# Kernel tuning notes

Measured on AMD Instinct MI355X. Metric: run time of the kernel, lower is better.

Reference implementation:

```python
import jax, jax.numpy as jnp
import numpy as np

CHUNK = 400
L = 50          # encoder kernel and stride
JUMP = CHUNK // L  # 8 new frames per streaming step
N = 128         # encoder feature dim
B = 128         # bottleneck dim
H = 512         # TCN hidden dim
K = 3           # depthwise kernel size
R, X = 2, 7     # repeats x blocks, dilations 2^0..2^6
BUF = 516       # ring buffer length: JUMP + 2*sum(dilations)*R = 8 + 508
EPS = 1e-8


def setup_inputs() -> dict:
    key = jax.random.key(0)
    ks = jax.random.split(key, 16)
    nb = R * X
    w = lambda i, shape: jax.random.normal(ks[i], shape, jnp.float32) * 0.05
    return dict(
        mixture=jax.random.normal(ks[0], (1, 2, CHUNK), jnp.float32),
        encoder_buffer=jax.random.uniform(ks[1], (1, N, BUF), dtype=jnp.float32),
        layernorm_buffer=jax.random.normal(ks[2], (1, B, BUF), jnp.float32),
        W_enc=w(3, (N, 2, L)),              # encoder Conv1d(2->N, k=L, s=L)
        ln_g=jnp.ones((N,), jnp.float32),    # channelwise LayerNorm affine
        ln_b=jnp.zeros((N,), jnp.float32),
        W_bn=w(4, (B, N)),                   # bottleneck 1x1 conv
        blk_w1=w(5, (nb, H, B)),             # per-block pointwise in
        blk_p1=jnp.full((nb,), 0.25, jnp.float32),
        blk_g1=jnp.ones((nb, H), jnp.float32),
        blk_b1=jnp.zeros((nb, H), jnp.float32),
        blk_dw=w(6, (nb, H, K)),             # depthwise dilated conv
        blk_p2=jnp.full((nb,), 0.25, jnp.float32),
        blk_g2=jnp.ones((nb, H), jnp.float32),
        blk_b2=jnp.zeros((nb, H), jnp.float32),
        blk_w2=w(7, (nb, B, H)),             # per-block pointwise out
        W_mask=w(8, (N, B)),                 # mask 1x1 conv (C=1 source)
        W_dec=w(9, (L, N)),                  # decoder basis Linear(N->L)
    )


def _cln(x, g, b):
    # channelwise LayerNorm: normalize over channel dim per time frame. x: [1,C,T]
    mu = jnp.mean(x, axis=1, keepdims=True)
    var = jnp.var(x, axis=1, keepdims=True)
    return g[None, :, None] * (x - mu) * jax.lax.rsqrt(var + EPS) + b[None, :, None]


def _prelu(x, a):
    return jnp.where(x >= 0, x, a * x)


def _dwconv(x, w, d):
    # valid dilated depthwise conv. x: [1,H,T], w: [H,K] -> [1,H,T-(K-1)*d]
    return jax.lax.conv_general_dilated(
        x, w[:, None, :], window_strides=(1,), padding='VALID',
        rhs_dilation=(d,), feature_group_count=H,
        dimension_numbers=('NCH', 'OIH', 'NCH'))


def reference(mixture, encoder_buffer, layernorm_buffer, W_enc, ln_g, ln_b, W_bn,
              blk_w1, blk_p1, blk_g1, blk_b1, blk_dw, blk_p2, blk_g2, blk_b2,
              blk_w2, W_mask, W_dec):
    # --- encoder: Conv1d(2->N, k=L, s=L) + ReLU -> JUMP new frames, ring-shift buffer
    enc = jax.nn.relu(jax.lax.conv_general_dilated(
        mixture, W_enc, window_strides=(L,), padding='VALID',
        dimension_numbers=('NCH', 'OIH', 'NCH')))          # [1,N,JUMP]
    encoder_buffer = jnp.concatenate([encoder_buffer[:, :, JUMP:], enc], axis=2)

    # --- separator front-end (network[0:2]): cLN + bottleneck 1x1, per-frame causal
    ln_new = jnp.einsum('oc,bct->bot', W_bn, _cln(enc, ln_g, ln_b))  # [1,B,JUMP]
    layernorm_buffer = jnp.concatenate([layernorm_buffer[:, :, JUMP:], ln_new], axis=2)

    # --- TCN (network[2]): valid causal dilated blocks, each shrinks time by 2*d
    x = layernorm_buffer                                   # [1,B,516]
    for i in range(R * X):
        d = 2 ** (i % X)
        y = jnp.einsum('hc,bct->bht', blk_w1[i], x)
        y = _cln(_prelu(y, blk_p1[i]), blk_g1[i], blk_b1[i])
        y = _dwconv(y, blk_dw[i], d)                       # time -= (K-1)*d
        y = _cln(_prelu(y, blk_p2[i]), blk_g2[i], blk_b2[i])
        y = jnp.einsum('ch,bht->bct', blk_w2[i], y)
        x = x[:, :, (K - 1) * d:] + y                      # residual on trailing frames
    # x: [1,B,JUMP]

    # --- mask conv (network[3]) + ReLU, reshape to [1,C=1,N,JUMP]
    mask = jax.nn.relu(jnp.einsum('nc,bct->bnt', W_mask, x)).reshape(1, 1, N, JUMP)

    # --- decoder: mask the newest JUMP encoder frames, basis Linear(N->L), stride=L
    src_w = encoder_buffer[:, None, :, -JUMP:] * mask      # [1,1,N,JUMP]
    est_source = jnp.einsum('ln,bcnt->bctl', W_dec, src_w).reshape(1, 1, JUMP * L)
    return est_source, encoder_buffer, layernorm_buffer
```

## Files before the change

kernel.cpp:

```cpp
#include <hip/hip_runtime.h>

#define CHUNK 400
#define LWIN 50
#define JUMP 8
#define NCH 128
#define BCH 128
#define HCH 512
#define NBLK 14
#define BUF 516
#define SHIFT 508
#define EPSV 1e-8f
#define NWG 136

typedef float f4v __attribute__((ext_vector_type(4)));

__device__ __forceinline__ void cstore4(float* p, float4 v) {
    f4v t = {v.x, v.y, v.z, v.w};
    asm volatile("global_store_dwordx4 %0, %1, off sc0 sc1"
                 :: "v"(p), "v"(t) : "memory");
}
__device__ __forceinline__ float4 cload4(const float* p) {
    f4v t;
    asm volatile("global_load_dwordx4 %0, %1, off sc0 sc1\n\ts_waitcnt vmcnt(0)"
                 : "=v"(t) : "v"(p) : "memory");
    return make_float4(t.x, t.y, t.z, t.w);
}
__device__ __forceinline__ void cload4x3(float4& a, float4& b, float4& c,
        const float* pa, const float* pb, const float* pc) {
    f4v ta, tb, tc;
    asm volatile("global_load_dwordx4 %0, %3, off sc0 sc1\n\t"
                 "global_load_dwordx4 %1, %4, off sc0 sc1\n\t"
                 "global_load_dwordx4 %2, %5, off sc0 sc1\n\t"
                 "s_waitcnt vmcnt(0)"
                 : "=&v"(ta), "=&v"(tb), "=&v"(tc)
                 : "v"(pa), "v"(pb), "v"(pc) : "memory");
    a = make_float4(ta.x, ta.y, ta.z, ta.w);
    b = make_float4(tb.x, tb.y, tb.z, tb.w);
    c = make_float4(tc.x, tc.y, tc.z, tc.w);
}
__device__ __forceinline__ void cstore(float* p, float v) {
    __hip_atomic_store(p, v, __ATOMIC_RELAXED, __HIP_MEMORY_SCOPE_AGENT);
}
__device__ __forceinline__ float cload(const float* p) {
    return __hip_atomic_load(p, __ATOMIC_RELAXED, __HIP_MEMORY_SCOPE_AGENT);
}

__device__ __forceinline__ void fwait(unsigned* flp, int base, int cnt, int tid) {
    if (tid < cnt) {
        unsigned* p = flp + base + tid;
        while (__hip_atomic_load(p, __ATOMIC_RELAXED, __HIP_MEMORY_SCOPE_AGENT) == 0)
            __builtin_amdgcn_s_sleep(1);
    }
    __syncthreads();
}
__device__ __forceinline__ void fset(unsigned* flp, int idx, int tid) {
    __syncthreads();
    if (tid == 0)
        __hip_atomic_store(flp + idx, 1u, __ATOMIC_RELAXED, __HIP_MEMORY_SCOPE_AGENT);
}

__device__ __forceinline__ void stage1_core(
    int tid, int lane, int wid, int t0, int nf,
    const float* __restrict__ w1b, float aPr,
    const float* __restrict__ gv, const float* __restrict__ bv,
    float* __restrict__ yout, float* redf, float* statsf,
    const float* xsv, float* ysT)
{
    float acc[4] = {0.f, 0.f, 0.f, 0.f};
    const float4* __restrict__ wr = (const float4*)(w1b + (size_t)tid * BCH);
    const float4* __restrict__ xv = (const float4*)xsv;
    #pragma unroll 4
    for (int c4 = 0; c4 < 32; ++c4) {
        float4 w = wr[c4];
        #pragma unroll
        for (int f = 0; f < 4; ++f) {
            float4 x = xv[f * 32 + c4];
            acc[f] += w.x * x.x + w.y * x.y + w.z * x.z + w.w * x.w;
        }
    }
    #pragma unroll
    for (int f = 0; f < 4; ++f) acc[f] = acc[f] >= 0.f ? acc[f] : aPr * acc[f];
    for (int f = 0; f < nf; ++f) {
        float s = acc[f], q = acc[f] * acc[f];
        #pragma unroll
        for (int o = 32; o; o >>= 1) { s += __shfl_xor(s, o); q += __shfl_xor(q, o); }
        if (lane == 0) { redf[(wid * 4 + f) * 2] = s; redf[(wid * 4 + f) * 2 + 1] = q; }
    }
    __syncthreads();
    if (tid < nf) {
        float s = 0.f, q = 0.f;
        #pragma unroll
        for (int w = 0; w < 8; ++w) { s += redf[(w * 4 + tid) * 2]; q += redf[(w * 4 + tid) * 2 + 1]; }
        float mean = s * (1.f / HCH);
        float var = q * (1.f / HCH) - mean * mean;
        statsf[tid * 2] = mean; statsf[tid * 2 + 1] = rsqrtf(var + EPSV);
    }
    __syncthreads();
    float gg = gv[tid], bb = bv[tid];
    for (int f = 0; f < nf; ++f)
        ysT[f * HCH + tid] = gg * (acc[f] - statsf[f * 2]) * statsf[f * 2 + 1] + bb;
    __syncthreads();
    int f2 = tid >> 7, h4 = tid & 127;
    if (f2 < nf)
        cstore4(&yout[(t0 + f2) * HCH + 4 * h4], *(float4*)&ysT[f2 * HCH + 4 * h4]);
}

__global__ __launch_bounds__(512) void k_fused(
    const float* __restrict__ mixture, const float* __restrict__ inEnc,
    const float* __restrict__ inLn, const float* __restrict__ Wenc,
    const float* __restrict__ lng, const float* __restrict__ lnb,
    const float* __restrict__ Wbn, const float* __restrict__ w1,
    const float* __restrict__ p1, const float* __restrict__ g1,
    const float* __restrict__ b1, const float* __restrict__ dwc,
    const float* __restrict__ p2, const float* __restrict__ g2,
    const float* __restrict__ b2, const float* __restrict__ w2,
    const float* __restrict__ Wmask, const float* __restrict__ Wdec,
    float* __restrict__ est, float* __restrict__ outEnc, float* __restrict__ outLn,
    unsigned* __restrict__ fl, float* __restrict__ enc,
    float* __restrict__ xbuf, float* __restrict__ ybuf)
{
    __shared__ float xs[4 * BCH];
    __shared__ float ys[4 * 528];
    __shared__ float redf[8 * 4 * 2];
    __shared__ float statsf[4 * 2];

    const int wg = blockIdx.x;
    const int tid = threadIdx.x;
    const int lane = tid & 63, wid = tid >> 6;
    const int j = wg;
    const size_t xstr = (size_t)BUF * BCH;
    const size_t ystr = (size_t)BUF * HCH;

    if (wg < 8) {
        int t = wg;
        float e = 0.f;
        if (tid < 128) {
            int c = tid;
            const float* w = Wenc + c * 100;
            const float* m = mixture + t * LWIN;
            #pragma unroll 10
            for (int l = 0; l < LWIN; ++l) e += m[l] * w[l] + m[CHUNK + l] * w[LWIN + l];
            e = fmaxf(e, 0.f);
            cstore(&enc[t * NCH + c], e);
            outEnc[c * BUF + SHIFT + t] = e;
            float s = e, q = e * e;
            #pragma unroll
            for (int o = 32; o; o >>= 1) { s += __shfl_xor(s, o); q += __shfl_xor(q, o); }
            if (lane == 0) { redf[(wid * 4) * 2] = s; redf[(wid * 4) * 2 + 1] = q; }
        }
        __syncthreads();
        if (tid < 128) {
            float S = redf[0] + redf[8], Q = redf[1] + redf[9];
            float mean = S * (1.f / NCH);
            float var = Q * (1.f / NCH) - mean * mean;
            float r = rsqrtf(var + EPSV);
            xs[tid] = lng[tid] * (e - mean) * r + lnb[tid];
        }
        __syncthreads();
        if (tid < 128) {
            float acc = 0.f;
            const float4* wr = (const float4*)(Wbn + tid * NCH);
            const float4* nv = (const float4*)xs;
            #pragma unroll 8
            for (int j4 = 0; j4 < 32; ++j4) {
                float4 w = wr[j4]; float4 x = nv[j4];
                acc += w.x * x.x + w.y * x.y + w.z * x.z + w.w * x.w;
            }
            outLn[tid * BUF + SHIFT + t] = acc;
            ys[tid] = acc;
        }
        __syncthreads();
        if (tid < 32)
            cstore4(&xbuf[(SHIFT + t) * BCH + 4 * tid], *(float4*)&ys[4 * tid]);
    } else {
        int ch = wg - 8;
        for (int t = tid; t < SHIFT; t += 512)
            outEnc[ch * BUF + t] = inEnc[ch * BUF + t + JUMP];
        if (ch < 127) {
            int f = tid >> 7, c = tid & 127;
            int t = 4 * ch + f;
            outLn[c * BUF + t] = inLn[c * BUF + t + JUMP];
        }
    }
    fset(fl, 0 * NWG + wg, tid);

    if (4 * j < BUF) {
        int t0 = 4 * j;
        if (j >= 127) {
            fwait(fl, (j == 127) ? 0 : 4, 4, tid);
            if (tid < 128) {
                float4 v = cload4(&xbuf[t0 * BCH + 4 * tid]);
                *(float4*)&xs[4 * tid] = v;
            }
        } else {
            int f = tid >> 7, c = tid & 127;
            xs[f * BCH + c] = inLn[c * BUF + t0 + f + JUMP];
        }
        __syncthreads();
        stage1_core(tid, lane, wid, t0, 4, w1, p1[0], g1, b1, ybuf, redf, statsf, xs, ys);
    }
    fset(fl, 1 * NWG + wg, tid);

    int T = BUF;
    for (int i = 0; i < NBLK; ++i) {
        const float* xin = xbuf + (size_t)(i & 1) * xstr;
        float* xout      = xbuf + (size_t)((i + 1) & 1) * xstr;
        const float* ycur = ybuf + (size_t)(i & 1) * ystr;
        float* ynext      = ybuf + (size_t)((i + 1) & 1) * ystr;
        int d = 1 << (i % 7);
        int Tout = T - 2 * d;
        int t0 = 4 * j;
        if (t0 < Tout) {
            int jmaxe = (T - 1) >> 2;
            int jmax = min(j + ((3 + 2 * d) >> 2), jmaxe);
            int woff = (i >= 1 && i < NBLK - 1) ? ((3 + 2 * (1 << ((i - 1) % 7))) >> 2) : 0;
            int jlo = max(0, j - woff);
            fwait(fl + (1 + i) * NWG, jlo, jmax - jlo + 1, tid);
            if (i == 0 && j >= 126) fwait(fl, 0, 8, tid);
            if (i == NBLK - 1) fwait(fl, 4 * j, 4, tid);
            int nf = min(4, Tout - t0);
            const int f = tid >> 7, h4 = tid & 127;
            float4 yv; yv.x = yv.y = yv.z = yv.w = 0.f;
            if (f < nf) {
                float4 ya, yb2, yc;
                cload4x3(ya, yb2, yc,
                         &ycur[(t0 + f) * HCH + 4 * h4],
                         &ycur[(t0 + f + d) * HCH + 4 * h4],
                         &ycur[(t0 + f + 2 * d) * HCH + 4 * h4]);
                const float* dwb = dwc + (size_t)i * HCH * 3 + 12 * h4;
                float4 w0 = *(const float4*)(dwb);
                float4 w1v = *(const float4*)(dwb + 4);
                float4 w2v = *(const float4*)(dwb + 8);
                float a2 = p2[i];
                yv.x = w0.x * ya.x + w0.y * yb2.x + w0.z * yc.x;
                yv.y = w0.w * ya.y + w1v.x * yb2.y + w1v.y * yc.y;
                yv.z = w1v.z * ya.z + w1v.w * yb2.z + w2v.x * yc.z;
                yv.w = w2v.y * ya.w + w2v.z * yb2.w + w2v.w * yc.w;
                yv.x = yv.x >= 0.f ? yv.x : a2 * yv.x;
                yv.y = yv.y >= 0.f ? yv.y : a2 * yv.y;
                yv.z = yv.z >= 0.f ? yv.z : a2 * yv.z;
                yv.w = yv.w >= 0.f ? yv.w : a2 * yv.w;
            }
            {
                float s = yv.x + yv.y + yv.z + yv.w;
                float q = yv.x * yv.x + yv.y * yv.y + yv.z * yv.z + yv.w * yv.w;
                #pragma unroll
                for (int o = 32; o; o >>= 1) { s += __shfl_xor(s, o); q += __shfl_xor(q, o); }
                if (lane == 0 && f < nf) { redf[wid * 2] = s; redf[wid * 2 + 1] = q; }
            }
            __syncthreads();
            if (tid < nf) {
                float s = redf[4 * tid] + redf[4 * tid + 2];
                float q = redf[4 * tid + 1] + redf[4 * tid + 3];
                float mean = s * (1.f / HCH);
                float var = q * (1.f / HCH) - mean * mean;
                statsf[tid * 2] = mean; statsf[tid * 2 + 1] = rsqrtf(var + EPSV);
            }
            __syncthreads();
            if (f < nf) {
                float mean = statsf[f * 2], rstd = statsf[f * 2 + 1];
                float4 gv = *(const float4*)&g2[i * HCH + 4 * h4];
                float4 bv = *(const float4*)&b2[i * HCH + 4 * h4];
                float4 nv;
                nv.x = gv.x * (yv.x - mean) * rstd + bv.x;
                nv.y = gv.y * (yv.y - mean) * rstd + bv.y;
                nv.z = gv.z * (yv.z - mean) * rstd + bv.z;
                nv.w = gv.w * (yv.w - mean) * rstd + bv.w;
                *(float4*)&ys[f * 528 + (h4 >> 5) * 132 + (h4 & 31) * 4] = nv;
            }
            __syncthreads();
            int c = tid >> 2, p = tid & 3;
            float acc[4] = {0.f, 0.f, 0.f, 0.f};
            const float4* wr = (const float4*)(w2 + (size_t)i * BCH * HCH + c * HCH + p * 128);
            const float* yb = ys + p * 132;
            #pragma unroll 4
            for (int j4 = 0; j4 < 32; ++j4) {
                float4 w = wr[j4];
                #pragma unroll
                for (int ff = 0; ff < 4; ++ff) {
                    float4 x = *(const float4*)&yb[ff * 528 + j4 * 4];
                    acc[ff] += w.x * x.x + w.y * x.y + w.z * x.z + w.w * x.w;
                }
            }
            for (int ff = 0; ff < nf; ++ff) {
                acc[ff] += __shfl_xor(acc[ff], 1);
                acc[ff] += __shfl_xor(acc[ff], 2);
            }
            if (p == 0)
                for (int ff = 0; ff < nf; ++ff) xs[ff * BCH + c] = acc[ff];
            __syncthreads();
            if (i == 0) {
                int f2 = tid >> 7, cc0 = tid & 127;
                if (f2 < nf) {
                    int t = t0 + f2 + 2;
                    float xr = (t <= 507) ? inLn[cc0 * BUF + t + JUMP]
                                          : cload(&xbuf[t * BCH + cc0]);
                    float xa = xs[f2 * BCH + cc0] + xr;
                    xs[f2 * BCH + cc0] = xa;
                    cstore(&xout[(t0 + f2) * BCH + cc0], xa);
                }
            } else if (tid < 128) {
                int f2 = tid >> 5, c4 = tid & 31;
                if (f2 < nf) {
                    float4 xr = cload4(&xin[(t0 + f2 + 2 * d) * BCH + 4 * c4]);
                    float4 xa = *(float4*)&xs[f2 * BCH + 4 * c4];
                    xa.x += xr.x; xa.y += xr.y; xa.z += xr.z; xa.w += xr.w;
                    *(float4*)&xs[f2 * BCH + 4 * c4] = xa;
                    cstore4(&xout[(t0 + f2) * BCH + 4 * c4], xa);
                }
            }
            __syncthreads();
            if (i < NBLK - 1) {
                stage1_core(tid, lane, wid, t0, nf,
                            w1 + (size_t)(i + 1) * HCH * BCH, p1[i + 1],
                            g1 + (i + 1) * HCH, b1 + (i + 1) * HCH, ynext,
                            redf, statsf, xs, ys);
            } else {
                int cc = tid & 127, f3 = tid >> 7;
                float m = 0.f;
                const float4* wm = (const float4*)(Wmask + cc * BCH);
                const float4* xv = (const float4*)(xs + f3 * BCH);
                #pragma unroll 8
                for (int j4 = 0; j4 < 32; ++j4) {
                    float4 w = wm[j4]; float4 x = xv[j4];
                    m += w.x * x.x + w.y * x.y + w.z * x.z + w.w * x.w;
                }
                m = fmaxf(m, 0.f);
                ys[f3 * BCH + cc] = m * cload(&enc[(t0 + f3) * NCH + cc]);
                __syncthreads();
                if (tid < 4 * LWIN) {
                    int ff = tid / LWIN, l = tid % LWIN;
                    float e = 0.f;
                    const float4* wd = (const float4*)(Wdec + l * NCH);
                    const float4* sv = (const float4*)(ys + ff * BCH);
                    #pragma unroll 8
                    for (int j4 = 0; j4 < 32; ++j4) {
                        float4 w = wd[j4]; float4 x = sv[j4];
                        e += w.x * x.x + w.y * x.y + w.z * x.z + w.w * x.w;
                    }
                    est[(t0 + ff) * LWIN + l] = e;
                }
            }
        }
        fset(fl, (2 + i) * NWG + wg, tid);
        T = Tout;
    }
}

extern "C" void kernel_launch(void* const* d_in, const int* in_sizes, int n_in,
                              void* d_out, int out_size, void* d_ws, size_t ws_size,
                              hipStream_t stream) {
    const float* mixture = (const float*)d_in[0];
    const float* inEnc   = (const float*)d_in[1];
    const float* inLn    = (const float*)d_in[2];
    const float* Wenc    = (const float*)d_in[3];
    const float* lng     = (const float*)d_in[4];
    const float* lnb     = (const float*)d_in[5];
    const float* Wbn     = (const float*)d_in[6];
    const float* w1      = (const float*)d_in[7];
    const float* p1      = (const float*)d_in[8];
    const float* g1      = (const float*)d_in[9];
    const float* b1      = (const float*)d_in[10];
    const float* dwc     = (const float*)d_in[11];
    const float* p2      = (const float*)d_in[12];
    const float* g2      = (const float*)d_in[13];
    const float* b2      = (const float*)d_in[14];
    const float* w2      = (const float*)d_in[15];
    const float* Wmask   = (const float*)d_in[16];
    const float* Wdec    = (const float*)d_in[17];

    float* est    = (float*)d_out;
    float* outEnc = est + CHUNK;
    float* outLn  = outEnc + NCH * BUF;

    unsigned* fl = (unsigned*)d_ws;
    float* enc  = (float*)d_ws + 2304;
    float* xbuf = enc + 1024;
    float* ybuf = xbuf + 2 * (size_t)BUF * BCH;

    (void)hipMemsetAsync(d_ws, 0, 9216, stream);

    void* args[] = { &mixture, &inEnc, &inLn, &Wenc, &lng, &lnb, &Wbn, &w1, &p1,
                     &g1, &b1, &dwc, &p2, &g2, &b2, &w2, &Wmask, &Wdec,
                     &est, &outEnc, &outLn, &fl, &enc, &xbuf, &ybuf };
    (void)hipLaunchCooperativeKernel((const void*)k_fused, dim3(NWG), dim3(512),
                                     (void**)args, 0, stream);
}
```

Measured before the change: 333.1 us.

## Triple-buffer TCN activations and wait only on exact dependency flags

When the workspace is large enough, the x/y ping-pong buffers become three-way rotating buffers. The per-block wait then polls only the producer flags the dilated conv actually reads (j, j+d/4, j+d/2 and so on) plus write-after-read guards from two blocks back, instead of a contiguous window of flags. This is meant to cut inter-workgroup stall time in the fine-grained flag synchronization. It adds workspace use, and the WAR dependency logic may be subtle.

```diff
diff --git a/kernel.cpp b/kernel.cpp
--- a/kernel.cpp
+++ b/kernel.cpp
@@ -45,12 +45,12 @@
     return __hip_atomic_load(p, __ATOMIC_RELAXED, __HIP_MEMORY_SCOPE_AGENT);
 }
 
+__device__ __forceinline__ void fpoll1(unsigned* p) {
+    while (__hip_atomic_load(p, __ATOMIC_RELAXED, __HIP_MEMORY_SCOPE_AGENT) == 0)
+        __builtin_amdgcn_s_sleep(1);
+}
 __device__ __forceinline__ void fwait(unsigned* flp, int base, int cnt, int tid) {
-    if (tid < cnt) {
-        unsigned* p = flp + base + tid;
-        while (__hip_atomic_load(p, __ATOMIC_RELAXED, __HIP_MEMORY_SCOPE_AGENT) == 0)
-            __builtin_amdgcn_s_sleep(1);
-    }
+    if (tid < cnt) fpoll1(flp + base + tid);
     __syncthreads();
 }
 __device__ __forceinline__ void fset(unsigned* flp, int idx, int tid) {
@@ -117,7 +117,7 @@
     const float* __restrict__ Wmask, const float* __restrict__ Wdec,
     float* __restrict__ est, float* __restrict__ outEnc, float* __restrict__ outLn,
     unsigned* __restrict__ fl, float* __restrict__ enc,
-    float* __restrict__ xbuf, float* __restrict__ ybuf)
+    float* __restrict__ xbuf, float* __restrict__ ybuf, int mode)
 {
     __shared__ float xs[4 * BCH];
     __shared__ float ys[4 * 528];
@@ -130,6 +130,7 @@
     const int j = wg;
     const size_t xstr = (size_t)BUF * BCH;
     const size_t ystr = (size_t)BUF * HCH;
+    const int ns = mode ? 3 : 2;
 
     if (wg < 8) {
         int t = wg;
@@ -203,21 +204,42 @@
 
     int T = BUF;
     for (int i = 0; i < NBLK; ++i) {
-        const float* xin = xbuf + (size_t)(i & 1) * xstr;
-        float* xout      = xbuf + (size_t)((i + 1) & 1) * xstr;
-        const float* ycur = ybuf + (size_t)(i & 1) * ystr;
-        float* ynext      = ybuf + (size_t)((i + 1) & 1) * ystr;
+        const float* xin = xbuf + (size_t)(i % ns) * xstr;
+        float* xout      = xbuf + (size_t)((i + 1) % ns) * xstr;
+        const float* ycur = ybuf + (size_t)(i % ns) * ystr;
+        float* ynext      = ybuf + (size_t)((i + 1) % ns) * ystr;
         int d = 1 << (i % 7);
         int Tout = T - 2 * d;
         int t0 = 4 * j;
         if (t0 < Tout) {
             int jmaxe = (T - 1) >> 2;
-            int jmax = min(j + ((3 + 2 * d) >> 2), jmaxe);
-            int woff = (i >= 1 && i < NBLK - 1) ? ((3 + 2 * (1 << ((i - 1) % 7))) >> 2) : 0;
-            int jlo = max(0, j - woff);
-            fwait(fl + (1 + i) * NWG, jlo, jmax - jlo + 1, tid);
-            if (i == 0 && j >= 126) fwait(fl, 0, 8, tid);
-            if (i == NBLK - 1) fwait(fl, 4 * j, 4, tid);
+            if (mode) {
+                unsigned* flv = fl + (1 + i) * NWG;
+                int tgt = -1;
+                if      (tid == 0) tgt = j;
+                else if (tid == 1) tgt = min(j + (d >> 2), jmaxe);
+                else if (tid == 2) tgt = min(j + ((d + 3) >> 2), jmaxe);
+                else if (tid == 3) tgt = min(j + (d >> 1), jmaxe);
+                else if (tid == 4) tgt = min(j + ((2 * d + 3) >> 2), jmaxe);
+                if (tgt >= 0) fpoll1(flv + tgt);
+                if (i >= 2) {
+                    int dm2 = 1 << ((i - 2) % 7);
+                    int wb = ((2 * dm2 + 3) >> 2) + 2;
+                    int jlo2 = max(0, j - wb);
+                    int cnt2 = j - jlo2;
+                    if (tid >= 8 && tid < 8 + cnt2) fpoll1(fl + i * NWG + jlo2 + (tid - 8));
+                }
+                if (i == 0 && j >= 126 && tid < 8) fpoll1(fl + tid);
+                if (i == NBLK - 1 && tid < 4) fpoll1(fl + 4 * j + tid);
+                __syncthreads();
+            } else {
+                int jmax = min(j + ((3 + 2 * d) >> 2), jmaxe);
+                int woff = (i >= 1 && i < NBLK - 1) ? ((3 + 2 * (1 << ((i - 1) % 7))) >> 2) : 0;
+                int jlo = max(0, j - woff);
+                fwait(fl + (1 + i) * NWG, jlo, jmax - jlo + 1, tid);
+                if (i == 0 && j >= 126) fwait(fl, 0, 8, tid);
+                if (i == NBLK - 1) fwait(fl, 4 * j, 4, tid);
+            }
             int nf = min(4, Tout - t0);
             const int f = tid >> 7, h4 = tid & 127;
             float4 yv; yv.x = yv.y = yv.z = yv.w = 0.f;
@@ -376,13 +398,20 @@
     unsigned* fl = (unsigned*)d_ws;
     float* enc  = (float*)d_ws + 2304;
     float* xbuf = enc + 1024;
-    float* ybuf = xbuf + 2 * (size_t)BUF * BCH;
+    const size_t xstr = (size_t)BUF * BCH;
+    const size_t ystr = (size_t)BUF * HCH;
+
+    int mode;
+    size_t need3 = (2304 + 1024 + 3 * xstr + 3 * ystr) * 4ull;
+    mode = (ws_size >= need3) ? 1 : 0;
+    int ns = mode ? 3 : 2;
+    float* ybuf = xbuf + (size_t)ns * xstr;
 
     (void)hipMemsetAsync(d_ws, 0, 9216, stream);
 
     void* args[] = { &mixture, &inEnc, &inLn, &Wenc, &lng, &lnb, &Wbn, &w1, &p1,
                      &g1, &b1, &dwc, &p2, &g2, &b2, &w2, &Wmask, &Wdec,
-                     &est, &outEnc, &outLn, &fl, &enc, &xbuf, &ybuf };
+                     &est, &outEnc, &outLn, &fl, &enc, &xbuf, &ybuf, &mode };
     (void)hipLaunchCooperativeKernel((const void*)k_fused, dim3(NWG), dim3(512),
                                      (void**)args, 0, stream);
 }
```

New measurement: 332.7 us. Within noise of the previous version (-0.1%).
